# Kernel tuning notes

Measured on AMD Instinct MI355X. Metric: run time of the kernel, lower is better.

## Reference

```python
import jax, jax.numpy as jnp
import numpy as np
import math

CTX_LEN = 2048
N_EMB = 256
HEAD_SIZE = 256
N_HEADS = 8
HEAD_DIM = HEAD_SIZE // N_HEADS  # 32
B, T = 4, 2048


def setup_inputs() -> dict:
    key = jax.random.key(0)
    k1, k2, k3, k4 = jax.random.split(key, 4)
    x = jax.random.normal(k1, (B, T, N_EMB), dtype=jnp.float32)
    # torch Linear(n_emb, 3*head_size, bias=False): store as [in, out] for x @ W
    w_attn = jax.random.normal(k2, (N_EMB, 3 * HEAD_SIZE), dtype=jnp.float32) * 0.02
    pos_embs = jax.random.normal(k3, (N_HEADS, CTX_LEN, HEAD_DIM), dtype=jnp.float32) * 0.02
    w_proj = jax.random.normal(k4, (HEAD_SIZE, N_EMB), dtype=jnp.float32) * 0.02
    b_proj = jnp.zeros((N_EMB,), dtype=jnp.float32)
    return {"x": x, "w_attn": w_attn, "pos_embs": pos_embs,
            "w_proj": w_proj, "b_proj": b_proj}


def reference(x, w_attn, pos_embs, w_proj, b_proj):
    Bsz, Tlen, _ = x.shape
    qkv = x @ w_attn                               # [B,T,3*HS]
    K, Q, V = jnp.split(qkv, 3, axis=-1)           # split order: K, Q, V (as in source)
    def heads(t):                                  # [B,T,HS] -> [B,H,T,hd]
        return t.reshape(Bsz, Tlen, N_HEADS, HEAD_DIM).transpose(0, 2, 1, 3)
    K, Q, V = heads(K), heads(Q), heads(V)

    # relative position term with skew trick
    pe = pos_embs[:, -Tlen:, :]                    # [H,T,hd]
    S_rel = jnp.einsum('bhtd,hsd->bhts', Q, pe)    # [B,H,T,T]
    flip_mask = jnp.flip(jnp.tril(jnp.ones((Tlen, Tlen), dtype=x.dtype)), axis=1)
    S_rel = S_rel * flip_mask
    # pad a zero column at the front, reshape [T+1,T], drop first row -> skew
    S_rel = jnp.pad(S_rel, ((0, 0), (0, 0), (0, 0), (1, 0)))
    S_rel = S_rel.reshape(Bsz, N_HEADS, Tlen + 1, Tlen)[:, :, 1:, :]

    scores = (jnp.einsum('bhtd,bhsd->bhts', Q, K) + S_rel) / math.sqrt(HEAD_DIM)
    causal = jnp.where(jnp.tril(jnp.ones((Tlen, Tlen), dtype=bool)), 0.0, -1e9).astype(x.dtype)
    scores = scores + causal
    attn = jax.nn.softmax(scores, axis=-1)         # dropout omitted (eval mode)

    out = jnp.einsum('bhts,bhsd->bhtd', attn, V)   # [B,H,T,hd]
    out = out.transpose(0, 2, 1, 3).reshape(Bsz, Tlen, HEAD_SIZE)
    return out @ w_proj + b_proj
```

## Files before the change

### kernel.cpp

```cpp
#include <hip/hip_runtime.h>
#include <math.h>

#define BB 4
#define TT 2048
#define TTP 2112
#define NEMB 256
#define NH 8
#define HD 32

typedef __attribute__((ext_vector_type(8))) short bf8;
typedef __attribute__((ext_vector_type(4))) float f4;

static __device__ __forceinline__ unsigned short f2bf(float f) {
    union { float f; unsigned u; } v; v.f = f;
    unsigned r = v.u + 0x7FFF + ((v.u >> 16) & 1);
    return (unsigned short)(r >> 16);
}
static __device__ __forceinline__ float bf2f(unsigned short s) {
    union { unsigned u; float f; } v; v.u = ((unsigned)s) << 16;
    return v.f;
}

template <int CTRL>
static __device__ __forceinline__ float dppmv(float x) {
    return __int_as_float(__builtin_amdgcn_mov_dpp(__float_as_int(x), CTRL, 0xF, 0xF, true));
}
static __device__ __forceinline__ float rowsum16(float x) {
    x += dppmv<0xB1>(x);
    x += dppmv<0x4E>(x);
    x += dppmv<0x124>(x);
    x += dppmv<0x128>(x);
    return x;
}

static __device__ __forceinline__ void tcvt_body(const float* __restrict__ src,
                                                 unsigned short* __restrict__ dst,
                                                 int R, int C, int gx, int gy,
                                                 float (*t)[65], int tid) {
    const int c0 = gx * 64, r0 = gy * 64;
    #pragma unroll
    for (int p = 0; p < 4; ++p) {
        const int i = tid + p * 256;
        const int r = i >> 4, c4 = (i & 15) * 4;
        const float4 v = *(const float4*)(src + (long)(r0 + r) * C + c0 + c4);
        t[r][c4] = v.x; t[r][c4+1] = v.y; t[r][c4+2] = v.z; t[r][c4+3] = v.w;
    }
    __syncthreads();
    #pragma unroll
    for (int p = 0; p < 4; ++p) {
        const int i = tid + p * 256;
        const int cr = i >> 4, r4 = (i & 15) * 4;
        ushort4 vv;
        vv.x = f2bf(t[r4+0][cr]); vv.y = f2bf(t[r4+1][cr]);
        vv.z = f2bf(t[r4+2][cr]); vv.w = f2bf(t[r4+3][cr]);
        *(ushort4*)(dst + (long)(c0 + cr) * R + r0 + r4) = vv;
    }
}

__global__ __launch_bounds__(256) void prep(const float* __restrict__ pe,
                                            unsigned short* __restrict__ peb,
                                            const float* __restrict__ wa,
                                            unsigned short* __restrict__ waT,
                                            const float* __restrict__ wp,
                                            unsigned short* __restrict__ wpT) {
    __shared__ float t[64][65];
    const int bx = blockIdx.x, tid = threadIdx.x;
    if (bx < 528) {
        const int idx4 = bx * 256 + tid;
        const int h   = idx4 / 16896;
        const int rem = idx4 - h * 16896;
        const int u   = rem >> 3;
        const int d4  = (rem & 7) * 4;
        ushort4 o = make_ushort4(0, 0, 0, 0);
        if (u < TT) {
            const float4 v = *(const float4*)(pe + ((long)(h * TT + u)) * HD + d4);
            o.x = f2bf(v.x); o.y = f2bf(v.y); o.z = f2bf(v.z); o.w = f2bf(v.w);
        }
        *(ushort4*)(peb + ((long)(h * TTP + u)) * HD + d4) = o;
    } else if (bx < 576) {
        const int lo = bx - 528;
        tcvt_body(wa, waT, 256, 768, lo % 12, lo / 12, t, tid);
    } else {
        const int lo = bx - 576;
        tcvt_body(wp, wpT, 256, 256, lo % 4, lo / 4, t, tid);
    }
}

__global__ __launch_bounds__(256) void qkv_mfma(const float* __restrict__ xg,
                                                const unsigned short* __restrict__ Bg,
                                                unsigned short* __restrict__ Kb,
                                                unsigned short* __restrict__ Qb,
                                                unsigned short* __restrict__ Vt) {
    __shared__ unsigned short sm[13824];
    unsigned short* As = sm;
    unsigned short* Bs = sm + 9216;
    const int tid = threadIdx.x;
    const int wv = tid >> 6, L = tid & 63;
    const int l15 = L & 15, q = L >> 4;
    const int n0 = blockIdx.x * 64;
    const int m0 = blockIdx.y * 128;

    f4 acc[2][4];
    #pragma unroll
    for (int mt = 0; mt < 2; ++mt)
        #pragma unroll
        for (int nt = 0; nt < 4; ++nt) acc[mt][nt] = (f4){0.f,0.f,0.f,0.f};

    for (int kc = 0; kc < 4; ++kc) {
        const int k0 = kc * 64;
        __syncthreads();
        #pragma unroll
        for (int p = 0; p < 4; ++p) {
            const int i = tid + p * 256;
            const int r = i >> 3, c = i & 7;
            const float4 va = *(const float4*)(xg + (long)(m0 + r) * 256 + k0 + c * 8);
            const float4 vb = *(const float4*)(xg + (long)(m0 + r) * 256 + k0 + c * 8 + 4);
            ushort4 lo, hi;
            lo.x = f2bf(va.x); lo.y = f2bf(va.y); lo.z = f2bf(va.z); lo.w = f2bf(va.w);
            hi.x = f2bf(vb.x); hi.y = f2bf(vb.y); hi.z = f2bf(vb.z); hi.w = f2bf(vb.w);
            *(ushort4*)(As + r * 72 + c * 8)     = lo;
            *(ushort4*)(As + r * 72 + c * 8 + 4) = hi;
        }
        #pragma unroll
        for (int p = 0; p < 2; ++p) {
            const int i = tid + p * 256;
            const int r = i >> 3, c = i & 7;
            *(bf8*)(Bs + r * 72 + c * 8) = *(const bf8*)(Bg + (long)(n0 + r) * 256 + k0 + c * 8);
        }
        __syncthreads();
        #pragma unroll
        for (int kk = 0; kk < 2; ++kk) {
            const bf8 a0 = *(const bf8*)(As + (wv * 32 + l15) * 72 + kk * 32 + q * 8);
            const bf8 a1 = *(const bf8*)(As + (wv * 32 + 16 + l15) * 72 + kk * 32 + q * 8);
            #pragma unroll
            for (int nt = 0; nt < 4; ++nt) {
                const bf8 bb = *(const bf8*)(Bs + (nt * 16 + l15) * 72 + kk * 32 + q * 8);
                acc[0][nt] = __builtin_amdgcn_mfma_f32_16x16x32_bf16(a0, bb, acc[0][nt], 0, 0, 0);
                acc[1][nt] = __builtin_amdgcn_mfma_f32_16x16x32_bf16(a1, bb, acc[1][nt], 0, 0, 0);
            }
        }
    }

    const int sec = n0 >> 8;
    #pragma unroll
    for (int mt = 0; mt < 2; ++mt) {
        const int gm = m0 + wv * 32 + mt * 16 + q * 4;
        const int b = gm >> 11, tb = gm & 2047;
        #pragma unroll
        for (int nt = 0; nt < 4; ++nt) {
            const int gn = n0 + nt * 16 + l15;
            const int cc = gn & 255, h = cc >> 5, d = cc & 31;
            const long bh = (long)b * NH + h;
            const f4 a = acc[mt][nt];
            if (sec == 2) {
                ushort4 vv;
                vv.x = f2bf(a[0]); vv.y = f2bf(a[1]); vv.z = f2bf(a[2]); vv.w = f2bf(a[3]);
                *(ushort4*)(Vt + (bh * HD + d) * TT + tb) = vv;
            } else if (sec == 1) {
                #pragma unroll
                for (int r = 0; r < 4; ++r)
                    Qb[(bh * TT + tb + r) * HD + d] = f2bf(a[r] * 0.25506655788696527f);
            } else {
                #pragma unroll
                for (int r = 0; r < 4; ++r)
                    Kb[(bh * TT + tb + r) * HD + d] = f2bf(a[r]);
            }
        }
    }
}

__global__ __launch_bounds__(256) void attn_kernel(const unsigned short* __restrict__ Kb,
                                                   const unsigned short* __restrict__ Qb,
                                                   const unsigned short* __restrict__ Vtg,
                                                   const unsigned short* __restrict__ peb,
                                                   unsigned short* __restrict__ po,
                                                   float* __restrict__ pl) {
    __shared__ unsigned short lds[14848];
    unsigned short* Ks  = lds;
    unsigned short* PEs = lds + 2560;
    unsigned short* Vts = lds + 7680;
    unsigned short* Psw = lds + 9984 + (threadIdx.x >> 6) * 1216;

    const int tid = threadIdx.x;
    const int wv  = tid >> 6;
    const int L   = tid & 63;
    const int l15 = L & 15;
    const int q   = L >> 4;
    const int pair = blockIdx.x >> 1;
    const int sblk = blockIdx.x & 1;
    const int h = blockIdx.y, b = blockIdx.z;
    const long bh = (long)b * NH + h;
    const unsigned short* Kg = Kb  + bh * TT * HD;
    const unsigned short* Qg = Qb  + bh * TT * HD;
    const unsigned short* Vg = Vtg + bh * HD * TT;
    const unsigned short* Pg = peb + (long)h * TTP * HD;

    const int krow = tid >> 2, kc = tid & 3;
    const int vrow = tid >> 3, vc = tid & 7;
    const f4 z4 = {0.f, 0.f, 0.f, 0.f};
    const f4 m4 = {-16.f, -16.f, -16.f, -16.f};

    int saddr[4]; unsigned pselL[4], pselX[4];
    #pragma unroll
    for (int r = 0; r < 4; ++r) {
        const int tcol = l15 + 15 - 4 * q - r;
        saddr[r] = ((q << 4) | (tcol & 15)) << 2;
        const bool c = tcol >= 16;
        pselL[r] = c ? 0x03020C0Cu : 0x01000C0Cu;
        pselX[r] = c ? 0x05040C0Cu : 0x03020C0Cu;
    }

    for (int half = 0; half < 2; ++half) {
        const int itile = half ? 31 - pair : pair;
        const int t0 = itile * 64;

        const bf8 aq = *(const bf8*)(Qg + (t0 + wv * 16 + l15) * HD + q * 8);
        f4 o0 = z4, o1 = z4;
        float l_st[4] = {0.f, 0.f, 0.f, 0.f};

        bf8 ck, cv, cp0, cp1;
        if (sblk <= itile) {
            const int s0 = sblk * 64;
            const int ub = TT - 64 - t0 + s0;
            ck  = *(const bf8*)(Kg + (s0 + krow) * HD + kc * 8);
            cv  = *(const bf8*)(Vg + vrow * TT + s0 + vc * 8);
            cp0 = *(const bf8*)(Pg + (long)(ub + krow) * HD + kc * 8);
            cp1 = *(const bf8*)(Pg + (long)(ub + 64 + krow) * HD + kc * 8);
        }

        for (int jt = sblk; jt <= itile; jt += 2) {
            __syncthreads();
            *(bf8*)(Ks  + krow * 40 + kc * 8)        = ck;
            *(bf8*)(Vts + vrow * 72 + vc * 8)        = cv;
            *(bf8*)(PEs + krow * 40 + kc * 8)        = cp0;
            *(bf8*)(PEs + (krow + 64) * 40 + kc * 8) = cp1;
            __syncthreads();

            if (jt + 2 <= itile) {
                const int s0n = (jt + 2) * 64;
                const int ubn = TT - 64 - t0 + s0n;
                ck  = *(const bf8*)(Kg + (s0n + krow) * HD + kc * 8);
                cv  = *(const bf8*)(Vg + vrow * TT + s0n + vc * 8);
                cp0 = *(const bf8*)(Pg + (long)(ubn + krow) * HD + kc * 8);
                cp1 = *(const bf8*)(Pg + (long)(ubn + 64 + krow) * HD + kc * 8);
            }

            f4 sa[4], ra[5];
            #pragma unroll
            for (int nt = 0; nt < 4; ++nt) {
                const bf8 bk = *(const bf8*)(Ks + (nt * 16 + l15) * 40 + q * 8);
                sa[nt] = __builtin_amdgcn_mfma_f32_16x16x32_bf16(aq, bk, m4, 0, 0, 0);
            }
            const int pebase = 48 - 16 * wv;
            #pragma unroll
            for (int nt = 0; nt < 5; ++nt) {
                const bf8 bp = *(const bf8*)(PEs + (pebase + nt * 16 + l15) * 40 + q * 8);
                ra[nt] = __builtin_amdgcn_mfma_f32_16x16x32_bf16(aq, bp, z4, 0, 0, 0);
            }

            #pragma unroll
            for (int r = 0; r < 4; ++r) {
                const unsigned w0 = __builtin_amdgcn_perm(
                    (unsigned)__float_as_int(ra[1][r]), (unsigned)__float_as_int(ra[0][r]), 0x07060302u);
                const unsigned w1 = __builtin_amdgcn_perm(
                    (unsigned)__float_as_int(ra[3][r]), (unsigned)__float_as_int(ra[2][r]), 0x07060302u);
                const unsigned w2 = ((unsigned)__float_as_int(ra[4][r])) >> 16;
                const int v0 = __builtin_amdgcn_ds_bpermute(saddr[r], (int)w0);
                const int v1 = __builtin_amdgcn_ds_bpermute(saddr[r], (int)w1);
                const int v2 = __builtin_amdgcn_ds_bpermute(saddr[r], (int)w2);
                sa[0][r] += __int_as_float((int)__builtin_amdgcn_perm((unsigned)v0, (unsigned)v0, pselL[r]));
                sa[1][r] += __int_as_float((int)__builtin_amdgcn_perm((unsigned)v1, (unsigned)v0, pselX[r]));
                sa[2][r] += __int_as_float((int)__builtin_amdgcn_perm((unsigned)v1, (unsigned)v1, pselL[r]));
                sa[3][r] += __int_as_float((int)__builtin_amdgcn_perm((unsigned)v2, (unsigned)v1, pselX[r]));
            }

            if (jt == itile) {
                #pragma unroll
                for (int nb = 0; nb < 4; ++nb)
                    #pragma unroll
                    for (int r = 0; r < 4; ++r) {
                        const int s_l = nb * 16 + l15;
                        const int t_l = wv * 16 + 4 * q + r;
                        if (s_l > t_l) sa[nb][r] = -1e30f;
                    }
            }

            #pragma unroll
            for (int r = 0; r < 4; ++r) {
                #pragma unroll
                for (int nb = 0; nb < 4; ++nb) {
                    const float p = exp2f(sa[nb][r]);
                    l_st[r] += p;
                    const unsigned pu = (unsigned)__float_as_int(p);
                    Psw[(4 * q + r) * 76 + nb * 16 + l15] =
                        (unsigned short)((pu + 0x8000u) >> 16);
                }
            }

            #pragma unroll
            for (int ks = 0; ks < 2; ++ks) {
                const bf8 ap  = *(const bf8*)(Psw + l15 * 76 + ks * 32 + q * 8);
                const bf8 bv0 = *(const bf8*)(Vts + l15 * 72 + ks * 32 + q * 8);
                const bf8 bv1 = *(const bf8*)(Vts + (16 + l15) * 72 + ks * 32 + q * 8);
                o0 = __builtin_amdgcn_mfma_f32_16x16x32_bf16(ap, bv0, o0, 0, 0, 0);
                o1 = __builtin_amdgcn_mfma_f32_16x16x32_bf16(ap, bv1, o1, 0, 0, 0);
            }
        }

        const long pt = (bh * 32 + itile) * 2 + sblk;
        unsigned short* pob = po + pt * 2048;
        #pragma unroll
        for (int r = 0; r < 4; ++r) {
            const int row = wv * 16 + 4 * q + r;
            pob[row * 32 + l15]      = f2bf(o0[r]);
            pob[row * 32 + 16 + l15] = f2bf(o1[r]);
            const float ls = rowsum16(l_st[r]);
            if (l15 == 0) pl[pt * 64 + row] = ls;
        }
    }
}

__global__ __launch_bounds__(256) void attn_merge(const unsigned short* __restrict__ po,
                                                  const float* __restrict__ pl,
                                                  unsigned short* __restrict__ attb) {
    const int i = blockIdx.x * 256 + threadIdx.x;
    const int d4   = i & 7;
    const int row  = (i >> 3) & 63;
    const int tile = (i >> 9) & 31;
    const int bh   = i >> 14;
    const int h = bh & 7, b = bh >> 3;
    const long pt0 = ((long)bh * 32 + tile) * 2;
    const float l0 = pl[pt0 * 64 + row], l1 = pl[(pt0 + 1) * 64 + row];
    const float inv = 1.0f / (l0 + l1);
    const ushort4 a = *(const ushort4*)(po + pt0 * 2048 + row * 32 + d4 * 4);
    const ushort4 c = *(const ushort4*)(po + (pt0 + 1) * 2048 + row * 32 + d4 * 4);
    ushort4 o;
    o.x = f2bf((bf2f(a.x) + bf2f(c.x)) * inv);
    o.y = f2bf((bf2f(a.y) + bf2f(c.y)) * inv);
    o.z = f2bf((bf2f(a.z) + bf2f(c.z)) * inv);
    o.w = f2bf((bf2f(a.w) + bf2f(c.w)) * inv);
    const int t = tile * 64 + row;
    *(ushort4*)(attb + ((long)(b * TT + t)) * NEMB + h * HD + d4 * 4) = o;
}

__global__ __launch_bounds__(256) void proj_mfma(const unsigned short* __restrict__ Ag,
                                                 const unsigned short* __restrict__ Bg,
                                                 const float* __restrict__ bias,
                                                 float* __restrict__ out) {
    __shared__ unsigned short sm[13824];
    unsigned short* As = sm;
    unsigned short* Bs = sm + 9216;
    const int tid = threadIdx.x;
    const int wv = tid >> 6, L = tid & 63;
    const int l15 = L & 15, q = L >> 4;
    const int n0 = blockIdx.x * 64;
    const int m0 = blockIdx.y * 128;

    f4 acc[2][4];
    #pragma unroll
    for (int mt = 0; mt < 2; ++mt)
        #pragma unroll
        for (int nt = 0; nt < 4; ++nt) acc[mt][nt] = (f4){0.f,0.f,0.f,0.f};

    for (int kc = 0; kc < 4; ++kc) {
        const int k0 = kc * 64;
        __syncthreads();
        #pragma unroll
        for (int p = 0; p < 4; ++p) {
            const int i = tid + p * 256;
            const int r = i >> 3, c = i & 7;
            *(bf8*)(As + r * 72 + c * 8) = *(const bf8*)(Ag + (long)(m0 + r) * 256 + k0 + c * 8);
        }
        #pragma unroll
        for (int p = 0; p < 2; ++p) {
            const int i = tid + p * 256;
            const int r = i >> 3, c = i & 7;
            *(bf8*)(Bs + r * 72 + c * 8) = *(const bf8*)(Bg + (long)(n0 + r) * 256 + k0 + c * 8);
        }
        __syncthreads();
        #pragma unroll
        for (int kk = 0; kk < 2; ++kk) {
            const bf8 a0 = *(const bf8*)(As + (wv * 32 + l15) * 72 + kk * 32 + q * 8);
            const bf8 a1 = *(const bf8*)(As + (wv * 32 + 16 + l15) * 72 + kk * 32 + q * 8);
            #pragma unroll
            for (int nt = 0; nt < 4; ++nt) {
                const bf8 bb = *(const bf8*)(Bs + (nt * 16 + l15) * 72 + kk * 32 + q * 8);
                acc[0][nt] = __builtin_amdgcn_mfma_f32_16x16x32_bf16(a0, bb, acc[0][nt], 0, 0, 0);
                acc[1][nt] = __builtin_amdgcn_mfma_f32_16x16x32_bf16(a1, bb, acc[1][nt], 0, 0, 0);
            }
        }
    }

    #pragma unroll
    for (int mt = 0; mt < 2; ++mt) {
        const int gm = m0 + wv * 32 + mt * 16 + q * 4;
        #pragma unroll
        for (int nt = 0; nt < 4; ++nt) {
            const int gn = n0 + nt * 16 + l15;
            const float bv = bias[gn];
            #pragma unroll
            for (int r = 0; r < 4; ++r)
                out[(long)(gm + r) * NEMB + gn] = acc[mt][nt][r] + bv;
        }
    }
}

extern "C" void kernel_launch(void* const* d_in, const int* in_sizes, int n_in,
                              void* d_out, int out_size, void* d_ws, size_t ws_size,
                              hipStream_t stream) {
    const float* x      = (const float*)d_in[0];
    const float* w_attn = (const float*)d_in[1];
    const float* pe     = (const float*)d_in[2];
    const float* w_proj = (const float*)d_in[3];
    const float* b_proj = (const float*)d_in[4];
    float* out = (float*)d_out;

    char* base = (char*)d_ws;
    unsigned short* Kb   = (unsigned short*)(base);
    unsigned short* Qb   = (unsigned short*)(base + ( 4u << 20));
    unsigned short* Vt   = (unsigned short*)(base + ( 8u << 20));
    unsigned short* attb = (unsigned short*)(base + (12u << 20));
    unsigned short* peb  = (unsigned short*)(base + (16u << 20));
    unsigned short* waT  = (unsigned short*)(base + (18u << 20));
    unsigned short* wpT  = (unsigned short*)(base + (37u << 19));
    unsigned short* po   = (unsigned short*)(base + (19u << 20));
    float*          pl   = (float*)        (base + (27u << 20));

    prep<<<dim3(592), 256, 0, stream>>>(pe, peb, w_attn, waT, w_proj, wpT);
    qkv_mfma<<<dim3(12, 64), 256, 0, stream>>>(x, waT, Kb, Qb, Vt);
    attn_kernel<<<dim3(32, NH, BB), 256, 0, stream>>>(Kb, Qb, Vt, peb, po, pl);
    attn_merge<<<dim3(2048), 256, 0, stream>>>(po, pl, attb);
    proj_mfma<<<dim3(4, 64), 256, 0, stream>>>(attb, wpT, b_proj, out);
}
```

Baseline: 156.2 us.

## Load K and PE MFMA operands directly from global; double-buffer V in LDS

K and relative-position embedding tiles are no longer staged through shared memory. Each wave now reads its MFMA B-operand fragments straight from global memory. Only the V tile stays in LDS, now double-buffered, so each iteration needs one barrier instead of two and LDS use shrinks. The cost is more global/L2 traffic, since each wave fetches its own K and PE fragments with no cross-wave reuse, and those loads are no longer prefetched an iteration ahead, which can expose latency.

```diff
diff --git a/kernel.cpp b/kernel.cpp
--- a/kernel.cpp
+++ b/kernel.cpp
@@ -175,11 +175,8 @@
                                                    const unsigned short* __restrict__ peb,
                                                    unsigned short* __restrict__ po,
                                                    float* __restrict__ pl) {
-    __shared__ unsigned short lds[14848];
-    unsigned short* Ks  = lds;
-    unsigned short* PEs = lds + 2560;
-    unsigned short* Vts = lds + 7680;
-    unsigned short* Psw = lds + 9984 + (threadIdx.x >> 6) * 1216;
+    __shared__ unsigned short lds[9472];
+    unsigned short* Psw = lds + 4608 + (threadIdx.x >> 6) * 1216;
 
     const int tid = threadIdx.x;
     const int wv  = tid >> 6;
@@ -195,7 +192,6 @@
     const unsigned short* Vg = Vtg + bh * HD * TT;
     const unsigned short* Pg = peb + (long)h * TTP * HD;
 
-    const int krow = tid >> 2, kc = tid & 3;
     const int vrow = tid >> 3, vc = tid & 7;
     const f4 z4 = {0.f, 0.f, 0.f, 0.f};
     const f4 m4 = {-16.f, -16.f, -16.f, -16.f};
@@ -218,45 +214,39 @@
         f4 o0 = z4, o1 = z4;
         float l_st[4] = {0.f, 0.f, 0.f, 0.f};
 
-        bf8 ck, cv, cp0, cp1;
-        if (sblk <= itile) {
-            const int s0 = sblk * 64;
-            const int ub = TT - 64 - t0 + s0;
-            ck  = *(const bf8*)(Kg + (s0 + krow) * HD + kc * 8);
-            cv  = *(const bf8*)(Vg + vrow * TT + s0 + vc * 8);
-            cp0 = *(const bf8*)(Pg + (long)(ub + krow) * HD + kc * 8);
-            cp1 = *(const bf8*)(Pg + (long)(ub + 64 + krow) * HD + kc * 8);
-        }
+        const bool any = (sblk <= itile);
+        int buf = 0;
+        if (any) {
+            const bf8 cv0 = *(const bf8*)(Vg + vrow * TT + sblk * 64 + vc * 8);
+            *(bf8*)(lds + vrow * 72 + vc * 8) = cv0;
+        }
+        __syncthreads();
 
         for (int jt = sblk; jt <= itile; jt += 2) {
-            __syncthreads();
-            *(bf8*)(Ks  + krow * 40 + kc * 8)        = ck;
-            *(bf8*)(Vts + vrow * 72 + vc * 8)        = cv;
-            *(bf8*)(PEs + krow * 40 + kc * 8)        = cp0;
-            *(bf8*)(PEs + (krow + 64) * 40 + kc * 8) = cp1;
-            __syncthreads();
-
-            if (jt + 2 <= itile) {
-                const int s0n = (jt + 2) * 64;
-                const int ubn = TT - 64 - t0 + s0n;
-                ck  = *(const bf8*)(Kg + (s0n + krow) * HD + kc * 8);
-                cv  = *(const bf8*)(Vg + vrow * TT + s0n + vc * 8);
-                cp0 = *(const bf8*)(Pg + (long)(ubn + krow) * HD + kc * 8);
-                cp1 = *(const bf8*)(Pg + (long)(ubn + 64 + krow) * HD + kc * 8);
-            }
-
-            f4 sa[4], ra[5];
-            #pragma unroll
-            for (int nt = 0; nt < 4; ++nt) {
-                const bf8 bk = *(const bf8*)(Ks + (nt * 16 + l15) * 40 + q * 8);
-                sa[nt] = __builtin_amdgcn_mfma_f32_16x16x32_bf16(aq, bk, m4, 0, 0, 0);
-            }
-            const int pebase = 48 - 16 * wv;
-            #pragma unroll
-            for (int nt = 0; nt < 5; ++nt) {
-                const bf8 bp = *(const bf8*)(PEs + (pebase + nt * 16 + l15) * 40 + q * 8);
-                ra[nt] = __builtin_amdgcn_mfma_f32_16x16x32_bf16(aq, bp, z4, 0, 0, 0);
-            }
+            const int s0 = jt * 64;
+
+            bf8 fk[4];
+            #pragma unroll
+            for (int nt = 0; nt < 4; ++nt)
+                fk[nt] = *(const bf8*)(Kg + (s0 + nt * 16 + l15) * HD + q * 8);
+            const int ub = TT - 64 - t0 + s0 + 48 - 16 * wv + l15;
+            bf8 fp[5];
+            #pragma unroll
+            for (int nt = 0; nt < 5; ++nt)
+                fp[nt] = *(const bf8*)(Pg + (long)(ub + nt * 16) * HD + q * 8);
+            const bool hn = (jt + 2 <= itile);
+            bf8 cvn;
+            if (hn) cvn = *(const bf8*)(Vg + vrow * TT + s0 + 128 + vc * 8);
+
+            f4 sa[4];
+            #pragma unroll
+            for (int nt = 0; nt < 4; ++nt)
+                sa[nt] = __builtin_amdgcn_mfma_f32_16x16x32_bf16(aq, fk[nt], m4, 0, 0, 0);
+
+            f4 ra[5];
+            #pragma unroll
+            for (int nt = 0; nt < 5; ++nt)
+                ra[nt] = __builtin_amdgcn_mfma_f32_16x16x32_bf16(aq, fp[nt], z4, 0, 0, 0);
 
             #pragma unroll
             for (int r = 0; r < 4; ++r) {
@@ -297,14 +287,19 @@
                 }
             }
 
+            const unsigned short* Vb = lds + buf * 2304;
             #pragma unroll
             for (int ks = 0; ks < 2; ++ks) {
                 const bf8 ap  = *(const bf8*)(Psw + l15 * 76 + ks * 32 + q * 8);
-                const bf8 bv0 = *(const bf8*)(Vts + l15 * 72 + ks * 32 + q * 8);
-                const bf8 bv1 = *(const bf8*)(Vts + (16 + l15) * 72 + ks * 32 + q * 8);
+                const bf8 bv0 = *(const bf8*)(Vb + l15 * 72 + ks * 32 + q * 8);
+                const bf8 bv1 = *(const bf8*)(Vb + (16 + l15) * 72 + ks * 32 + q * 8);
                 o0 = __builtin_amdgcn_mfma_f32_16x16x32_bf16(ap, bv0, o0, 0, 0, 0);
                 o1 = __builtin_amdgcn_mfma_f32_16x16x32_bf16(ap, bv1, o1, 0, 0, 0);
             }
+
+            if (hn) *(bf8*)(lds + (buf ^ 1) * 2304 + vrow * 72 + vc * 8) = cvn;
+            __syncthreads();
+            buf ^= 1;
         }
 
         const long pt = (bh * 32 + itile) * 2 + sblk;
```

Result: slower. 167.5 us (+7.2%).

## Launch one block per query tile heaviest-first and drop register prefetch

Applied to the files above, without the earlier changes.

Replaces the paired light/heavy query-tile scheme (one block handling tile p and 31-p) with one block per (query tile, key-parity) launched in descending tile order, doubling the grid to 2048 blocks. The register-based prefetch of the next K/V/PE tile is removed in favour of direct global-to-LDS loads each iteration. This aims to improve load balance and occupancy by relying on the hardware scheduler and LPT ordering, at the cost of exposed global-load latency per iteration.

```diff
diff --git a/kernel.cpp b/kernel.cpp
--- a/kernel.cpp
+++ b/kernel.cpp
@@ -186,8 +186,8 @@
     const int L   = tid & 63;
     const int l15 = L & 15;
     const int q   = L >> 4;
-    const int pair = blockIdx.x >> 1;
-    const int sblk = blockIdx.x & 1;
+    const int itile = 31 - (blockIdx.x >> 1);
+    const int sblk  = blockIdx.x & 1;
     const int h = blockIdx.y, b = blockIdx.z;
     const long bh = (long)b * NH + h;
     const unsigned short* Kg = Kb  + bh * TT * HD;
@@ -210,113 +210,96 @@
         pselX[r] = c ? 0x05040C0Cu : 0x03020C0Cu;
     }
 
-    for (int half = 0; half < 2; ++half) {
-        const int itile = half ? 31 - pair : pair;
-        const int t0 = itile * 64;
-
-        const bf8 aq = *(const bf8*)(Qg + (t0 + wv * 16 + l15) * HD + q * 8);
-        f4 o0 = z4, o1 = z4;
-        float l_st[4] = {0.f, 0.f, 0.f, 0.f};
-
-        bf8 ck, cv, cp0, cp1;
-        if (sblk <= itile) {
-            const int s0 = sblk * 64;
-            const int ub = TT - 64 - t0 + s0;
-            ck  = *(const bf8*)(Kg + (s0 + krow) * HD + kc * 8);
-            cv  = *(const bf8*)(Vg + vrow * TT + s0 + vc * 8);
-            cp0 = *(const bf8*)(Pg + (long)(ub + krow) * HD + kc * 8);
-            cp1 = *(const bf8*)(Pg + (long)(ub + 64 + krow) * HD + kc * 8);
-        }
-
-        for (int jt = sblk; jt <= itile; jt += 2) {
-            __syncthreads();
-            *(bf8*)(Ks  + krow * 40 + kc * 8)        = ck;
-            *(bf8*)(Vts + vrow * 72 + vc * 8)        = cv;
-            *(bf8*)(PEs + krow * 40 + kc * 8)        = cp0;
-            *(bf8*)(PEs + (krow + 64) * 40 + kc * 8) = cp1;
-            __syncthreads();
-
-            if (jt + 2 <= itile) {
-                const int s0n = (jt + 2) * 64;
-                const int ubn = TT - 64 - t0 + s0n;
-                ck  = *(const bf8*)(Kg + (s0n + krow) * HD + kc * 8);
-                cv  = *(const bf8*)(Vg + vrow * TT + s0n + vc * 8);
-                cp0 = *(const bf8*)(Pg + (long)(ubn + krow) * HD + kc * 8);
-                cp1 = *(const bf8*)(Pg + (long)(ubn + 64 + krow) * HD + kc * 8);
+    const int t0 = itile * 64;
+    const bf8 aq = *(const bf8*)(Qg + (t0 + wv * 16 + l15) * HD + q * 8);
+    f4 o0 = z4, o1 = z4;
+    float l_st[4] = {0.f, 0.f, 0.f, 0.f};
+
+    for (int jt = sblk; jt <= itile; jt += 2) {
+        const int s0 = jt * 64;
+        const int ubase = TT - 64 - t0 + s0;
+        __syncthreads();
+        *(bf8*)(Ks  + krow * 40 + kc * 8) = *(const bf8*)(Kg + (s0 + krow) * HD + kc * 8);
+        *(bf8*)(Vts + vrow * 72 + vc * 8) = *(const bf8*)(Vg + vrow * TT + s0 + vc * 8);
+        #pragma unroll
+        for (int kk = 0; kk < 2; ++kk) {
+            const int i  = tid + kk * 256;
+            const int pr = i >> 2, pc = i & 3;
+            *(bf8*)(PEs + pr * 40 + pc * 8) = *(const bf8*)(Pg + (long)(ubase + pr) * HD + pc * 8);
+        }
+        __syncthreads();
+
+        f4 sa[4], ra[5];
+        #pragma unroll
+        for (int nt = 0; nt < 4; ++nt) {
+            const bf8 bk = *(const bf8*)(Ks + (nt * 16 + l15) * 40 + q * 8);
+            sa[nt] = __builtin_amdgcn_mfma_f32_16x16x32_bf16(aq, bk, m4, 0, 0, 0);
+        }
+        const int pebase = 48 - 16 * wv;
+        #pragma unroll
+        for (int nt = 0; nt < 5; ++nt) {
+            const bf8 bp = *(const bf8*)(PEs + (pebase + nt * 16 + l15) * 40 + q * 8);
+            ra[nt] = __builtin_amdgcn_mfma_f32_16x16x32_bf16(aq, bp, z4, 0, 0, 0);
+        }
+
+        #pragma unroll
+        for (int r = 0; r < 4; ++r) {
+            const unsigned w0 = __builtin_amdgcn_perm(
+                (unsigned)__float_as_int(ra[1][r]), (unsigned)__float_as_int(ra[0][r]), 0x07060302u);
+            const unsigned w1 = __builtin_amdgcn_perm(
+                (unsigned)__float_as_int(ra[3][r]), (unsigned)__float_as_int(ra[2][r]), 0x07060302u);
+            const unsigned w2 = ((unsigned)__float_as_int(ra[4][r])) >> 16;
+            const int v0 = __builtin_amdgcn_ds_bpermute(saddr[r], (int)w0);
+            const int v1 = __builtin_amdgcn_ds_bpermute(saddr[r], (int)w1);
+            const int v2 = __builtin_amdgcn_ds_bpermute(saddr[r], (int)w2);
+            sa[0][r] += __int_as_float((int)__builtin_amdgcn_perm((unsigned)v0, (unsigned)v0, pselL[r]));
+            sa[1][r] += __int_as_float((int)__builtin_amdgcn_perm((unsigned)v1, (unsigned)v0, pselX[r]));
+            sa[2][r] += __int_as_float((int)__builtin_amdgcn_perm((unsigned)v1, (unsigned)v1, pselL[r]));
+            sa[3][r] += __int_as_float((int)__builtin_amdgcn_perm((unsigned)v2, (unsigned)v1, pselX[r]));
+        }
+
+        if (jt == itile) {
+            #pragma unroll
+            for (int nb = 0; nb < 4; ++nb)
+                #pragma unroll
+                for (int r = 0; r < 4; ++r) {
+                    const int s_l = nb * 16 + l15;
+                    const int t_l = wv * 16 + 4 * q + r;
+                    if (s_l > t_l) sa[nb][r] = -1e30f;
+                }
+        }
+
+        #pragma unroll
+        for (int r = 0; r < 4; ++r) {
+            #pragma unroll
+            for (int nb = 0; nb < 4; ++nb) {
+                const float p = exp2f(sa[nb][r]);
+                l_st[r] += p;
+                const unsigned pu = (unsigned)__float_as_int(p);
+                Psw[(4 * q + r) * 76 + nb * 16 + l15] =
+                    (unsigned short)((pu + 0x8000u) >> 16);
             }
-
-            f4 sa[4], ra[5];
-            #pragma unroll
-            for (int nt = 0; nt < 4; ++nt) {
-                const bf8 bk = *(const bf8*)(Ks + (nt * 16 + l15) * 40 + q * 8);
-                sa[nt] = __builtin_amdgcn_mfma_f32_16x16x32_bf16(aq, bk, m4, 0, 0, 0);
-            }
-            const int pebase = 48 - 16 * wv;
-            #pragma unroll
-            for (int nt = 0; nt < 5; ++nt) {
-                const bf8 bp = *(const bf8*)(PEs + (pebase + nt * 16 + l15) * 40 + q * 8);
-                ra[nt] = __builtin_amdgcn_mfma_f32_16x16x32_bf16(aq, bp, z4, 0, 0, 0);
-            }
-
-            #pragma unroll
-            for (int r = 0; r < 4; ++r) {
-                const unsigned w0 = __builtin_amdgcn_perm(
-                    (unsigned)__float_as_int(ra[1][r]), (unsigned)__float_as_int(ra[0][r]), 0x07060302u);
-                const unsigned w1 = __builtin_amdgcn_perm(
-                    (unsigned)__float_as_int(ra[3][r]), (unsigned)__float_as_int(ra[2][r]), 0x07060302u);
-                const unsigned w2 = ((unsigned)__float_as_int(ra[4][r])) >> 16;
-                const int v0 = __builtin_amdgcn_ds_bpermute(saddr[r], (int)w0);
-                const int v1 = __builtin_amdgcn_ds_bpermute(saddr[r], (int)w1);
-                const int v2 = __builtin_amdgcn_ds_bpermute(saddr[r], (int)w2);
-                sa[0][r] += __int_as_float((int)__builtin_amdgcn_perm((unsigned)v0, (unsigned)v0, pselL[r]));
-                sa[1][r] += __int_as_float((int)__builtin_amdgcn_perm((unsigned)v1, (unsigned)v0, pselX[r]));
-                sa[2][r] += __int_as_float((int)__builtin_amdgcn_perm((unsigned)v1, (unsigned)v1, pselL[r]));
-                sa[3][r] += __int_as_float((int)__builtin_amdgcn_perm((unsigned)v2, (unsigned)v1, pselX[r]));
-            }
-
-            if (jt == itile) {
-                #pragma unroll
-                for (int nb = 0; nb < 4; ++nb)
-                    #pragma unroll
-                    for (int r = 0; r < 4; ++r) {
-                        const int s_l = nb * 16 + l15;
-                        const int t_l = wv * 16 + 4 * q + r;
-                        if (s_l > t_l) sa[nb][r] = -1e30f;
-                    }
-            }
-
-            #pragma unroll
-            for (int r = 0; r < 4; ++r) {
-                #pragma unroll
-                for (int nb = 0; nb < 4; ++nb) {
-                    const float p = exp2f(sa[nb][r]);
-                    l_st[r] += p;
-                    const unsigned pu = (unsigned)__float_as_int(p);
-                    Psw[(4 * q + r) * 76 + nb * 16 + l15] =
-                        (unsigned short)((pu + 0x8000u) >> 16);
-                }
-            }
-
-            #pragma unroll
-            for (int ks = 0; ks < 2; ++ks) {
-                const bf8 ap  = *(const bf8*)(Psw + l15 * 76 + ks * 32 + q * 8);
-                const bf8 bv0 = *(const bf8*)(Vts + l15 * 72 + ks * 32 + q * 8);
-                const bf8 bv1 = *(const bf8*)(Vts + (16 + l15) * 72 + ks * 32 + q * 8);
-                o0 = __builtin_amdgcn_mfma_f32_16x16x32_bf16(ap, bv0, o0, 0, 0, 0);
-                o1 = __builtin_amdgcn_mfma_f32_16x16x32_bf16(ap, bv1, o1, 0, 0, 0);
-            }
-        }
-
-        const long pt = (bh * 32 + itile) * 2 + sblk;
-        unsigned short* pob = po + pt * 2048;
-        #pragma unroll
-        for (int r = 0; r < 4; ++r) {
-            const int row = wv * 16 + 4 * q + r;
-            pob[row * 32 + l15]      = f2bf(o0[r]);
-            pob[row * 32 + 16 + l15] = f2bf(o1[r]);
-            const float ls = rowsum16(l_st[r]);
-            if (l15 == 0) pl[pt * 64 + row] = ls;
-        }
+        }
+
+        #pragma unroll
+        for (int ks = 0; ks < 2; ++ks) {
+            const bf8 ap  = *(const bf8*)(Psw + l15 * 76 + ks * 32 + q * 8);
+            const bf8 bv0 = *(const bf8*)(Vts + l15 * 72 + ks * 32 + q * 8);
+            const bf8 bv1 = *(const bf8*)(Vts + (16 + l15) * 72 + ks * 32 + q * 8);
+            o0 = __builtin_amdgcn_mfma_f32_16x16x32_bf16(ap, bv0, o0, 0, 0, 0);
+            o1 = __builtin_amdgcn_mfma_f32_16x16x32_bf16(ap, bv1, o1, 0, 0, 0);
+        }
+    }
+
+    const long pt = (bh * 32 + itile) * 2 + sblk;
+    unsigned short* pob = po + pt * 2048;
+    #pragma unroll
+    for (int r = 0; r < 4; ++r) {
+        const int row = wv * 16 + 4 * q + r;
+        pob[row * 32 + l15]      = f2bf(o0[r]);
+        pob[row * 32 + 16 + l15] = f2bf(o1[r]);
+        const float ls = rowsum16(l_st[r]);
+        if (l15 == 0) pl[pt * 64 + row] = ls;
     }
 }
 
@@ -428,7 +411,7 @@
 
     prep<<<dim3(592), 256, 0, stream>>>(pe, peb, w_attn, waT, w_proj, wpT);
     qkv_mfma<<<dim3(12, 64), 256, 0, stream>>>(x, waT, Kb, Qb, Vt);
-    attn_kernel<<<dim3(32, NH, BB), 256, 0, stream>>>(Kb, Qb, Vt, peb, po, pl);
+    attn_kernel<<<dim3(64, NH, BB), 256, 0, stream>>>(Kb, Qb, Vt, peb, po, pl);
     attn_merge<<<dim3(2048), 256, 0, stream>>>(po, pl, attb);
     proj_mfma<<<dim3(4, 64), 256, 0, stream>>>(attb, wpT, b_proj, out);
 }
```

New measurement: 187.0 us. 19.7% more time.
